# Performance work log

Hardware: AMD Instinct MI355X
Metric: run time of the kernel (lower is better)

## Reference

```python
import jax, jax.numpy as jnp
import numpy as np

EPS = 0.01  # Normalizer eps
N_NODES = 100000
N_EDGES = 1600000


def gcn_conv(x, edge_index, W, b, n_nodes):
    """PyG-style GCNConv: x @ W, symmetric-normalized aggregation with self-loops, + bias."""
    src = jnp.concatenate([edge_index[0], jnp.arange(n_nodes)])  # [E+N]
    dst = jnp.concatenate([edge_index[1], jnp.arange(n_nodes)])  # [E+N]
    h = x @ W  # [N, out]
    ones = jnp.ones_like(dst, dtype=h.dtype)
    deg = jax.ops.segment_sum(ones, dst, num_segments=n_nodes)  # [N]
    dinv = jnp.where(deg > 0, jax.lax.rsqrt(deg), 0.0)
    norm = dinv[src] * dinv[dst]  # [E+N]
    msgs = h[src] * norm[:, None]  # [E+N, out]  (largest intermediate)
    out = jax.ops.segment_sum(msgs, dst, num_segments=n_nodes)  # [N, out]
    return out + b


def setup_inputs() -> dict:
    key = jax.random.key(0)
    k = jax.random.split(key, 6)
    x = jax.random.normal(k[0], (N_NODES, 16), dtype=jnp.float32)
    edge_index = jax.random.randint(k[1], (2, N_EDGES), 0, N_NODES)
    W1 = jax.random.normal(k[2], (16, 64), dtype=jnp.float32) * 0.25
    b1 = jax.random.normal(k[3], (64,), dtype=jnp.float32) * 0.1
    W3 = jax.random.normal(k[4], (64, 32), dtype=jnp.float32) * 0.125
    b3 = jax.random.normal(k[5], (32,), dtype=jnp.float32) * 0.1
    return {"x": x, "edge_index": edge_index, "W1": W1, "b1": b1, "W3": W3, "b3": b3}


def reference(x, edge_index, W1, b1, W3, b3):
    n = x.shape[0]
    h = jax.nn.relu(gcn_conv(x, edge_index, W1, b1, n))
    h = jax.nn.relu(gcn_conv(h, edge_index, W3, b3, n))
    # Normalizer: sequential Welford observe over all nodes then normalize with
    # FINAL stats == population mean / clamped population variance.
    mean = h.mean(axis=0)  # [32]
    var = jnp.maximum(((h - mean) ** 2).mean(axis=0), EPS)  # [32]
    return (h - mean) * jax.lax.rsqrt(var)
```

## Files before the change

kernel.cpp:

```cpp
#include <hip/hip_runtime.h>
#include <hip/hip_fp16.h>

#define EPS 0.01f
#define SCAN_BS 512
#define NCHUNKS 256
#define BUCKET_SHIFT 9
#define BUCKET_SZ (1 << BUCKET_SHIFT)


__global__ __launch_bounds__(SCAN_BS) void k_scan_block(const int* __restrict__ in,
                                                        int* __restrict__ out,
                                                        int* __restrict__ bsum, int n) {
    __shared__ int sd[SCAN_BS];
    int t = threadIdx.x;
    int gid = blockIdx.x * SCAN_BS + t;
    int v = (gid < n) ? in[gid] : 0;
    sd[t] = v;
    __syncthreads();
    for (int off = 1; off < SCAN_BS; off <<= 1) {
        int x = (t >= off) ? sd[t - off] : 0;
        __syncthreads();
        sd[t] += x;
        __syncthreads();
    }
    if (gid < n) out[gid] = sd[t] - v;
    if (t == SCAN_BS - 1) bsum[blockIdx.x] = sd[t];
}

__global__ __launch_bounds__(SCAN_BS) void k_scan_tops(int* __restrict__ bsum, int nb) {
    __shared__ int sd[SCAN_BS];
    int t = threadIdx.x;
    int v = (t < nb) ? bsum[t] : 0;
    sd[t] = v;
    __syncthreads();
    for (int off = 1; off < SCAN_BS; off <<= 1) {
        int x = (t >= off) ? sd[t - off] : 0;
        __syncthreads();
        sd[t] += x;
        __syncthreads();
    }
    if (t < nb) bsum[t] = sd[t] - v;
}

__global__ __launch_bounds__(SCAN_BS) void k_scan_add(int* __restrict__ out,
                                                      const int* __restrict__ bsum, int n) {
    int gid = blockIdx.x * SCAN_BS + threadIdx.x;
    if (gid < n) out[gid] += bsum[blockIdx.x];
}


__global__ __launch_bounds__(256) void kA_bucket_hist(const int* __restrict__ dst,
                                                      int* __restrict__ bh, int e,
                                                      int nbuck, int ce) {
    extern __shared__ int hist[];
    int b = blockIdx.x, t = threadIdx.x;
    for (int i = t; i < nbuck; i += 256) hist[i] = 0;
    __syncthreads();
    int lo = b * ce, hi = min(lo + ce, e);
    for (int i = lo + t; i < hi; i += 256) atomicAdd(&hist[dst[i] >> BUCKET_SHIFT], 1);
    __syncthreads();
    for (int i = t; i < nbuck; i += 256) bh[i * NCHUNKS + b] = hist[i];
}

__global__ __launch_bounds__(256) void kC_bucket_scatter(const int* __restrict__ src,
                                                         const int* __restrict__ dst,
                                                         const int* __restrict__ bhs,
                                                         unsigned int* __restrict__ eb, int e,
                                                         int nbuck, int ce) {
    extern __shared__ int cur[];
    int b = blockIdx.x, t = threadIdx.x;
    for (int i = t; i < nbuck; i += 256) cur[i] = bhs[i * NCHUNKS + b];
    __syncthreads();
    int lo = b * ce, hi = min(lo + ce, e);
    for (int i = lo + t; i < hi; i += 256) {
        int s = src[i], d = dst[i];
        int pos = atomicAdd(&cur[d >> BUCKET_SHIFT], 1);
        eb[pos] = ((unsigned int)(d & (BUCKET_SZ - 1)) << 23) | (unsigned int)s;
    }
}

__global__ __launch_bounds__(256) void kDeg(const unsigned int* __restrict__ eb,
                                            const int* __restrict__ bhs,
                                            int* __restrict__ degi,
                                            int n, int nbuck, int e) {
    __shared__ int hist[BUCKET_SZ];
    int k = blockIdx.x, t = threadIdx.x;
    for (int i = t; i < BUCKET_SZ; i += 256) hist[i] = 0;
    __syncthreads();
    int lo = bhs[k * NCHUNKS];
    int hi = (k + 1 < nbuck) ? bhs[(k + 1) * NCHUNKS] : e;
    for (int i = lo + t; i < hi; i += 256) atomicAdd(&hist[eb[i] >> 23], 1);
    __syncthreads();
    int node0 = k << BUCKET_SHIFT;
    for (int i = t; i < BUCKET_SZ; i += 256) {
        int node = node0 + i;
        if (node < n) degi[node] = hist[i];
    }
}

__global__ void k_dinv(const int* __restrict__ degi, float* __restrict__ dinv, int n) {
    int i = blockIdx.x * blockDim.x + threadIdx.x;
    if (i < n) dinv[i] = rsqrtf((float)degi[i] + 1.0f);
}

__global__ __launch_bounds__(256) void kD_fill(const unsigned int* __restrict__ eb,
                                               const int* __restrict__ bhs,
                                               const int* __restrict__ rowstart,
                                               int* __restrict__ csr_src,
                                               int n, int nbuck, int e) {
    __shared__ int cur[BUCKET_SZ];
    int k = blockIdx.x, t = threadIdx.x;
    int node0 = k << BUCKET_SHIFT;
    for (int i = t; i < BUCKET_SZ; i += 256) {
        int node = node0 + i;
        cur[i] = (node < n) ? rowstart[node] : 0;
    }
    __syncthreads();
    int lo = bhs[k * NCHUNKS];
    int hi = (k + 1 < nbuck) ? bhs[(k + 1) * NCHUNKS] : e;
    for (int i = lo + t; i < hi; i += 256) {
        unsigned int p = eb[i];
        int dl = (int)(p >> 23);
        int s = (int)(p & 0x7fffffu);
        int pos = atomicAdd(&cur[dl], 1);
        csr_src[pos] = s;
    }
}


__global__ __launch_bounds__(256) void k_prescale16(const float* __restrict__ x,
                                                    const float* __restrict__ dinv,
                                                    __half* __restrict__ xs, int n) {
    long long idx = (long long)blockIdx.x * 256 + threadIdx.x;
    if (idx < (long long)n * 16) {
        int row = (int)(idx >> 4);
        xs[idx] = __float2half(x[idx] * dinv[row]);
    }
}


__global__ __launch_bounds__(256) void k_l1_fused(const int* __restrict__ rowstart,
                                                  const int* __restrict__ degi,
                                                  const int* __restrict__ csr_src,
                                                  const float* __restrict__ dinv,
                                                  const __half* __restrict__ xs,
                                                  const float* __restrict__ W1,
                                                  const float* __restrict__ b1,
                                                  const float* __restrict__ W3,
                                                  __half* __restrict__ h2s, int n) {
    __shared__ float w1[16 * 64];
    __shared__ float w3[64 * 32];
    __shared__ float bs[64];
    __shared__ __align__(16) float a[16 * 16];
    __shared__ float z[16 * 64];
    int t = threadIdx.x;
    for (int i = t; i < 16 * 64; i += 256) w1[i] = W1[i];
    for (int i = t; i < 64 * 32; i += 256) w3[i] = W3[i];
    if (t < 64) bs[t] = b1[t];

    int row0 = blockIdx.x * 16;
    int wv = t >> 6;
    int lane = t & 63;
    int c2 = lane & 7;
    int slot = lane >> 3;
    const __half2* xs2 = (const __half2*)xs;

    for (int nid = 0; nid < 4; ++nid) {
        int node = row0 + wv * 4 + nid;
        if (node < n) {
            const int* sp = csr_src + rowstart[node];
            int deg = degi[node];
            float ax = 0.f, ay = 0.f, bx = 0.f, by = 0.f;
            int k = slot;
            for (; k + 8 < deg; k += 16) {
                int s0 = sp[k], s1 = sp[k + 8];
                float2 v0 = __half22float2(xs2[(size_t)s0 * 8 + c2]);
                float2 v1 = __half22float2(xs2[(size_t)s1 * 8 + c2]);
                ax += v0.x; ay += v0.y;
                bx += v1.x; by += v1.y;
            }
            if (k < deg) {
                int s0 = sp[k];
                float2 v0 = __half22float2(xs2[(size_t)s0 * 8 + c2]);
                ax += v0.x; ay += v0.y;
            }
            float sx = ax + bx, sy = ay + by;
            sx += __shfl_xor(sx, 8);  sy += __shfl_xor(sy, 8);
            sx += __shfl_xor(sx, 16); sy += __shfl_xor(sy, 16);
            sx += __shfl_xor(sx, 32); sy += __shfl_xor(sy, 32);
            if (slot == 0) {
                float2 self = __half22float2(xs2[(size_t)node * 8 + c2]);
                float dn = dinv[node];
                int r = wv * 4 + nid;
                ((float2*)(a + r * 16))[c2] = make_float2(dn * (sx + self.x), dn * (sy + self.y));
            }
        }
    }
    __syncthreads();

    for (int i = t; i < 1024; i += 256) {
        int r = i >> 6, c = i & 63;
        float acc = bs[c];
#pragma unroll
        for (int k = 0; k < 16; ++k) acc += a[r * 16 + k] * w1[k * 64 + c];
        z[i] = acc > 0.f ? acc : 0.f;
    }
    __syncthreads();
    for (int i = t; i < 512; i += 256) {
        int r = i >> 5, c = i & 31;
        float acc = 0.f;
#pragma unroll
        for (int k = 0; k < 64; ++k) acc += z[r * 64 + k] * w3[k * 32 + c];
        int row = row0 + r;
        if (row < n) h2s[(size_t)row * 32 + c] = __float2half(acc * dinv[row]);
    }
}


__global__ __launch_bounds__(256) void k_gather32_stats(const int* __restrict__ rowstart,
                                                        const int* __restrict__ degi,
                                                        const int* __restrict__ csr_src,
                                                        const float* __restrict__ dinv,
                                                        const __half* __restrict__ h2s,
                                                        const float* __restrict__ b3,
                                                        float* __restrict__ out,
                                                        float* __restrict__ partial, int n) {
    int t = threadIdx.x;
    int lane = t & 63;
    int c2 = lane & 15;
    int slot = lane >> 4;
    const __half2* h2 = (const __half2*)h2s;
    float2 bias = ((const float2*)b3)[c2];
    float s_x = 0.f, s_y = 0.f, q_x = 0.f, q_y = 0.f;
    for (int it = 0; it < 8; ++it) {
        int node = blockIdx.x * 32 + it * 4 + (t >> 6);
        if (node < n) {
            const int* sp = csr_src + rowstart[node];
            int deg = degi[node];
            float ax = 0.f, ay = 0.f, bx = 0.f, by = 0.f;
            int k = slot;
            for (; k + 4 < deg; k += 8) {
                int s0 = sp[k], s1 = sp[k + 4];
                float2 v0 = __half22float2(h2[(size_t)s0 * 16 + c2]);
                float2 v1 = __half22float2(h2[(size_t)s1 * 16 + c2]);
                ax += v0.x; ay += v0.y;
                bx += v1.x; by += v1.y;
            }
            if (k < deg) {
                int s0 = sp[k];
                float2 v0 = __half22float2(h2[(size_t)s0 * 16 + c2]);
                ax += v0.x; ay += v0.y;
            }
            float sx = ax + bx, sy = ay + by;
            sx += __shfl_xor(sx, 16); sy += __shfl_xor(sy, 16);
            sx += __shfl_xor(sx, 32); sy += __shfl_xor(sy, 32);
            if (slot == 0) {
                float2 self = __half22float2(h2[(size_t)node * 16 + c2]);
                float dn = dinv[node];
                float vx = dn * (sx + self.x) + bias.x;
                float vy = dn * (sy + self.y) + bias.y;
                vx = vx > 0.f ? vx : 0.f;
                vy = vy > 0.f ? vy : 0.f;
                ((float2*)(out + (size_t)node * 32))[c2] = make_float2(vx, vy);
                s_x += vx; s_y += vy;
                q_x += vx * vx; q_y += vy * vy;
            }
        }
    }
    __shared__ float ls[128], lq[128];
    int wv = t >> 6;
    if ((t & 63) < 16) {
        ls[wv * 32 + 2 * c2] = s_x;
        ls[wv * 32 + 2 * c2 + 1] = s_y;
        lq[wv * 32 + 2 * c2] = q_x;
        lq[wv * 32 + 2 * c2 + 1] = q_y;
    }
    __syncthreads();
    if (t < 32) {
        float a = 0.f, b = 0.f;
#pragma unroll
        for (int w = 0; w < 4; ++w) {
            a += ls[w * 32 + t];
            b += lq[w * 32 + t];
        }
        atomicAdd(&partial[t], a);
        atomicAdd(&partial[32 + t], b);
    }
}


__global__ void k_zero_partials(float* __restrict__ p) {
    int t = threadIdx.x;
    if (t < 64) p[t] = 0.f;
}

__global__ void k_finalize(const float* __restrict__ partial, float* __restrict__ meaninv, int n) {
    int t = threadIdx.x;
    if (t < 32) {
        float invn = 1.0f / (float)n;
        float mean = partial[t] * invn;
        float var = partial[32 + t] * invn - mean * mean;
        var = var > EPS ? var : EPS;
        meaninv[t] = mean;
        meaninv[32 + t] = rsqrtf(var);
    }
}

__global__ void k_norm(float* __restrict__ h, const float* __restrict__ meaninv, int n) {
    long long idx = (long long)blockIdx.x * blockDim.x + threadIdx.x;
    if (idx < (long long)n * 32) {
        int c = (int)(idx & 31);
        h[idx] = (h[idx] - meaninv[c]) * meaninv[32 + c];
    }
}

extern "C" void kernel_launch(void* const* d_in, const int* in_sizes, int n_in,
                              void* d_out, int out_size, void* d_ws, size_t ws_size,
                              hipStream_t stream) {
    const float* x  = (const float*)d_in[0];
    const int* ei   = (const int*)d_in[1];
    const float* W1 = (const float*)d_in[2];
    const float* b1 = (const float*)d_in[3];
    const float* W3 = (const float*)d_in[4];
    const float* b3 = (const float*)d_in[5];

    const int N = in_sizes[0] / 16;
    const int E = in_sizes[1] / 2;
    const int* src = ei;
    const int* dst = ei + E;

    const int NBUCK = (N + BUCKET_SZ - 1) >> BUCKET_SHIFT;
    const int CE = (E + NCHUNKS - 1) / NCHUNKS;
    const int BH_TOTAL = NBUCK * NCHUNKS;

    char* ws = (char*)d_ws;
    int*   degi     = (int*)ws;          ws += (size_t)N * 4;
    float* dinv     = (float*)ws;        ws += (size_t)N * 4;
    int*   rowstart = (int*)ws;          ws += (size_t)N * 4;
    int*   bsum     = (int*)ws;          ws += (size_t)SCAN_BS * 4;
    int*   bsum2    = (int*)ws;          ws += (size_t)SCAN_BS * 4;
    int*   bh       = (int*)ws;          ws += (size_t)BH_TOTAL * 4;
    int*   bhs      = (int*)ws;          ws += (size_t)BH_TOTAL * 4;
    unsigned int* eb = (unsigned int*)ws; ws += (size_t)E * 4;
    int*   csr_src  = (int*)ws;          ws += (size_t)E * 4;
    __half* xs      = (__half*)ws;       ws += (size_t)N * 16 * 2;
    __half* h2s     = (__half*)ws;       ws += (size_t)N * 32 * 2;
    float* partial  = (float*)ws;        ws += 64 * 4;
    float* meaninv  = (float*)ws;

    float* out = (float*)d_out;

    const int NB = (N + SCAN_BS - 1) / SCAN_BS;
    const int NB2 = (BH_TOTAL + SCAN_BS - 1) / SCAN_BS;

    kA_bucket_hist<<<NCHUNKS, 256, NBUCK * 4, stream>>>(dst, bh, E, NBUCK, CE);
    k_scan_block<<<NB2, SCAN_BS, 0, stream>>>(bh, bhs, bsum2, BH_TOTAL);
    k_scan_tops<<<1, SCAN_BS, 0, stream>>>(bsum2, NB2);
    k_scan_add<<<NB2, SCAN_BS, 0, stream>>>(bhs, bsum2, BH_TOTAL);
    kC_bucket_scatter<<<NCHUNKS, 256, NBUCK * 4, stream>>>(src, dst, bhs, eb, E, NBUCK, CE);

    kDeg<<<NBUCK, 256, 0, stream>>>(eb, bhs, degi, N, NBUCK, E);
    k_dinv<<<(N + 255) / 256, 256, 0, stream>>>(degi, dinv, N);
    k_scan_block<<<NB, SCAN_BS, 0, stream>>>(degi, rowstart, bsum, N);
    k_scan_tops<<<1, SCAN_BS, 0, stream>>>(bsum, NB);
    k_scan_add<<<NB, SCAN_BS, 0, stream>>>(rowstart, bsum, N);
    kD_fill<<<NBUCK, 256, 0, stream>>>(eb, bhs, rowstart, csr_src, N, NBUCK, E);

    k_prescale16<<<((long long)N * 16 + 255) / 256, 256, 0, stream>>>(x, dinv, xs, N);
    k_l1_fused<<<(N + 15) / 16, 256, 0, stream>>>(rowstart, degi, csr_src, dinv, xs,
                                                  W1, b1, W3, h2s, N);

    k_zero_partials<<<1, 64, 0, stream>>>(partial);
    k_gather32_stats<<<(N + 31) / 32, 256, 0, stream>>>(rowstart, degi, csr_src, dinv, h2s,
                                                        b3, out, partial, N);

    k_finalize<<<1, 64, 0, stream>>>(partial, meaninv, N);
    k_norm<<<((long long)N * 32 + 255) / 256, 256, 0, stream>>>(out, meaninv, N);
}
```

Before: 198.1 us.

## Fuse degree, rowstart scan, dinv and prescale into bucket kernel; contiguous gather slices

Replaces the degree kernel, dinv kernel, three-kernel global rowstart scan, prescale kernel and partials zeroing with one per-bucket kernel. Rowstart comes from the bucket offset plus a local block scan, because edges are already grouped by destination bucket. The gather loops in both layers now give each slot a contiguous slice of neighbours instead of a strided one, and layer 2 unrolls by four. This cuts six launches and some global traffic, at the cost of fewer blocks for the prescale work and possibly uneven slice lengths per slot.

```diff
diff --git a/kernel.cpp b/kernel.cpp
--- a/kernel.cpp
+++ b/kernel.cpp
@@ -79,28 +79,60 @@
     }
 }
 
-__global__ __launch_bounds__(256) void kDeg(const unsigned int* __restrict__ eb,
-                                            const int* __restrict__ bhs,
-                                            int* __restrict__ degi,
-                                            int n, int nbuck, int e) {
+__global__ __launch_bounds__(256) void kDeg_scan_prescale(const unsigned int* __restrict__ eb,
+                                                          const int* __restrict__ bhs,
+                                                          const float* __restrict__ x,
+                                                          int* __restrict__ degi,
+                                                          float* __restrict__ dinv,
+                                                          int* __restrict__ rowstart,
+                                                          __half* __restrict__ xs,
+                                                          float* __restrict__ partial,
+                                                          int n, int nbuck, int e) {
     __shared__ int hist[BUCKET_SZ];
+    __shared__ int ps[256];
+    __shared__ float dv[BUCKET_SZ];
     int k = blockIdx.x, t = threadIdx.x;
+    if (k == 0 && t < 64) partial[t] = 0.f;
     for (int i = t; i < BUCKET_SZ; i += 256) hist[i] = 0;
     __syncthreads();
     int lo = bhs[k * NCHUNKS];
     int hi = (k + 1 < nbuck) ? bhs[(k + 1) * NCHUNKS] : e;
     for (int i = lo + t; i < hi; i += 256) atomicAdd(&hist[eb[i] >> 23], 1);
     __syncthreads();
+    int a0 = hist[2 * t], a1 = hist[2 * t + 1];
+    ps[t] = a0 + a1;
+    __syncthreads();
+    for (int off = 1; off < 256; off <<= 1) {
+        int v = (t >= off) ? ps[t - off] : 0;
+        __syncthreads();
+        ps[t] += v;
+        __syncthreads();
+    }
+    int excl = ps[t] - (a0 + a1);
     int node0 = k << BUCKET_SHIFT;
-    for (int i = t; i < BUCKET_SZ; i += 256) {
-        int node = node0 + i;
-        if (node < n) degi[node] = hist[i];
-    }
-}
-
-__global__ void k_dinv(const int* __restrict__ degi, float* __restrict__ dinv, int n) {
-    int i = blockIdx.x * blockDim.x + threadIdx.x;
-    if (i < n) dinv[i] = rsqrtf((float)degi[i] + 1.0f);
+    {
+        int nd0 = node0 + 2 * t, nd1 = nd0 + 1;
+        float d0 = rsqrtf((float)a0 + 1.0f);
+        float d1 = rsqrtf((float)a1 + 1.0f);
+        dv[2 * t] = d0;
+        dv[2 * t + 1] = d1;
+        if (nd0 < n) {
+            degi[nd0] = a0;
+            dinv[nd0] = d0;
+            rowstart[nd0] = lo + excl;
+        }
+        if (nd1 < n) {
+            degi[nd1] = a1;
+            dinv[nd1] = d1;
+            rowstart[nd1] = lo + excl + a0;
+        }
+    }
+    __syncthreads();
+    for (int i = t; i < BUCKET_SZ * 16; i += 256) {
+        int rl = i >> 4;
+        int node = node0 + rl;
+        if (node < n) xs[(size_t)node * 16 + (i & 15)] = __float2half(x[(size_t)node * 16 + (i & 15)] * dv[rl]);
+    }
 }
 
 __global__ __launch_bounds__(256) void kD_fill(const unsigned int* __restrict__ eb,
@@ -124,17 +156,6 @@
         int s = (int)(p & 0x7fffffu);
         int pos = atomicAdd(&cur[dl], 1);
         csr_src[pos] = s;
-    }
-}
-
-
-__global__ __launch_bounds__(256) void k_prescale16(const float* __restrict__ x,
-                                                    const float* __restrict__ dinv,
-                                                    __half* __restrict__ xs, int n) {
-    long long idx = (long long)blockIdx.x * 256 + threadIdx.x;
-    if (idx < (long long)n * 16) {
-        int row = (int)(idx >> 4);
-        xs[idx] = __float2half(x[idx] * dinv[row]);
     }
 }
 
@@ -170,16 +191,19 @@
         if (node < n) {
             const int* sp = csr_src + rowstart[node];
             int deg = degi[node];
+            int L = (deg + 7) >> 3;
+            int base = slot * L;
+            int end = min(base + L, deg);
             float ax = 0.f, ay = 0.f, bx = 0.f, by = 0.f;
-            int k = slot;
-            for (; k + 8 < deg; k += 16) {
-                int s0 = sp[k], s1 = sp[k + 8];
+            int k = base;
+            for (; k + 2 <= end; k += 2) {
+                int s0 = sp[k], s1 = sp[k + 1];
                 float2 v0 = __half22float2(xs2[(size_t)s0 * 8 + c2]);
                 float2 v1 = __half22float2(xs2[(size_t)s1 * 8 + c2]);
                 ax += v0.x; ay += v0.y;
                 bx += v1.x; by += v1.y;
             }
-            if (k < deg) {
+            if (k < end) {
                 int s0 = sp[k];
                 float2 v0 = __half22float2(xs2[(size_t)s0 * 8 + c2]);
                 ax += v0.x; ay += v0.y;
@@ -237,21 +261,30 @@
         if (node < n) {
             const int* sp = csr_src + rowstart[node];
             int deg = degi[node];
+            int L = (deg + 3) >> 2;
+            int base = slot * L;
+            int end = min(base + L, deg);
             float ax = 0.f, ay = 0.f, bx = 0.f, by = 0.f;
-            int k = slot;
-            for (; k + 4 < deg; k += 8) {
-                int s0 = sp[k], s1 = sp[k + 4];
+            float cx = 0.f, cy = 0.f, dx = 0.f, dy = 0.f;
+            int k = base;
+            for (; k + 4 <= end; k += 4) {
+                int s0 = sp[k], s1 = sp[k + 1], s2 = sp[k + 2], s3 = sp[k + 3];
                 float2 v0 = __half22float2(h2[(size_t)s0 * 16 + c2]);
                 float2 v1 = __half22float2(h2[(size_t)s1 * 16 + c2]);
+                float2 v2 = __half22float2(h2[(size_t)s2 * 16 + c2]);
+                float2 v3 = __half22float2(h2[(size_t)s3 * 16 + c2]);
                 ax += v0.x; ay += v0.y;
                 bx += v1.x; by += v1.y;
-            }
-            if (k < deg) {
+                cx += v2.x; cy += v2.y;
+                dx += v3.x; dy += v3.y;
+            }
+            for (; k < end; ++k) {
                 int s0 = sp[k];
                 float2 v0 = __half22float2(h2[(size_t)s0 * 16 + c2]);
                 ax += v0.x; ay += v0.y;
             }
-            float sx = ax + bx, sy = ay + by;
+            float sx = (ax + bx) + (cx + dx);
+            float sy = (ay + by) + (cy + dy);
             sx += __shfl_xor(sx, 16); sy += __shfl_xor(sy, 16);
             sx += __shfl_xor(sx, 32); sy += __shfl_xor(sy, 32);
             if (slot == 0) {
@@ -289,11 +322,6 @@
 }
 
 
-__global__ void k_zero_partials(float* __restrict__ p) {
-    int t = threadIdx.x;
-    if (t < 64) p[t] = 0.f;
-}
-
 __global__ void k_finalize(const float* __restrict__ partial, float* __restrict__ meaninv, int n) {
     int t = threadIdx.x;
     if (t < 32) {
@@ -337,7 +365,6 @@
     int*   degi     = (int*)ws;          ws += (size_t)N * 4;
     float* dinv     = (float*)ws;        ws += (size_t)N * 4;
     int*   rowstart = (int*)ws;          ws += (size_t)N * 4;
-    int*   bsum     = (int*)ws;          ws += (size_t)SCAN_BS * 4;
     int*   bsum2    = (int*)ws;          ws += (size_t)SCAN_BS * 4;
     int*   bh       = (int*)ws;          ws += (size_t)BH_TOTAL * 4;
     int*   bhs      = (int*)ws;          ws += (size_t)BH_TOTAL * 4;
@@ -350,7 +377,6 @@
 
     float* out = (float*)d_out;
 
-    const int NB = (N + SCAN_BS - 1) / SCAN_BS;
     const int NB2 = (BH_TOTAL + SCAN_BS - 1) / SCAN_BS;
 
     kA_bucket_hist<<<NCHUNKS, 256, NBUCK * 4, stream>>>(dst, bh, E, NBUCK, CE);
@@ -359,18 +385,13 @@
     k_scan_add<<<NB2, SCAN_BS, 0, stream>>>(bhs, bsum2, BH_TOTAL);
     kC_bucket_scatter<<<NCHUNKS, 256, NBUCK * 4, stream>>>(src, dst, bhs, eb, E, NBUCK, CE);
 
-    kDeg<<<NBUCK, 256, 0, stream>>>(eb, bhs, degi, N, NBUCK, E);
-    k_dinv<<<(N + 255) / 256, 256, 0, stream>>>(degi, dinv, N);
-    k_scan_block<<<NB, SCAN_BS, 0, stream>>>(degi, rowstart, bsum, N);
-    k_scan_tops<<<1, SCAN_BS, 0, stream>>>(bsum, NB);
-    k_scan_add<<<NB, SCAN_BS, 0, stream>>>(rowstart, bsum, N);
+    kDeg_scan_prescale<<<NBUCK, 256, 0, stream>>>(eb, bhs, x, degi, dinv, rowstart, xs,
+                                                  partial, N, NBUCK, E);
     kD_fill<<<NBUCK, 256, 0, stream>>>(eb, bhs, rowstart, csr_src, N, NBUCK, E);
 
-    k_prescale16<<<((long long)N * 16 + 255) / 256, 256, 0, stream>>>(x, dinv, xs, N);
     k_l1_fused<<<(N + 15) / 16, 256, 0, stream>>>(rowstart, degi, csr_src, dinv, xs,
                                                   W1, b1, W3, h2s, N);
 
-    k_zero_partials<<<1, 64, 0, stream>>>(partial);
     k_gather32_stats<<<(N + 31) / 32, 256, 0, stream>>>(rowstart, degi, csr_src, dinv, h2s,
                                                         b3, out, partial, N);
 
```

Result: no change. 194.6 us (-1.8%).
